# Kernel tuning notes

Hardware: AMD Instinct MI355X
Metric: run time of the kernel (lower is better)

## Reference

```python
import jax, jax.numpy as jnp
import numpy as np

NUM_HEADS = 16
THETA = 10000.0


def _rope(x, cos, sin):
    # x: [B, H, S, d_k]; cos/sin: [S, d_k//2] broadcast over B, H
    x1 = x[..., 0::2]
    x2 = x[..., 1::2]
    r1 = cos * x1 - sin * x2
    r2 = sin * x1 + cos * x2
    # interleave back: (..., half_d, 2) -> (..., d_k)
    return jnp.stack((r1, r2), axis=-1).reshape(x.shape)


def setup_inputs() -> dict:
    key = jax.random.key(0)
    ks = jax.random.split(key, 5)
    B, S, D = 4, 2048, 1024
    scale = D ** -0.5
    x = jax.random.normal(ks[0], (B, S, D), dtype=jnp.float32)
    wq = jax.random.normal(ks[1], (D, D), dtype=jnp.float32) * scale
    wk = jax.random.normal(ks[2], (D, D), dtype=jnp.float32) * scale
    wv = jax.random.normal(ks[3], (D, D), dtype=jnp.float32) * scale
    wo = jax.random.normal(ks[4], (D, D), dtype=jnp.float32) * scale
    return {"x": x, "wq": wq, "wk": wk, "wv": wv, "wo": wo}


def reference(x, wq, wk, wv, wo):
    B, S, D = x.shape
    H = NUM_HEADS
    dk = D // H

    def proj(w):
        # x @ w.T, split heads -> [B, H, S, dk]
        y = jnp.einsum('bsd,ed->bse', x, w)
        return y.reshape(B, S, H, dk).transpose(0, 2, 1, 3)

    q, k, v = proj(wq), proj(wk), proj(wv)

    # RoPE (interleaved pairs), positions = arange(S)
    inv_freq = THETA ** (-(jnp.arange(0, dk, 2, dtype=jnp.float32) / dk))
    ang = jnp.arange(S, dtype=jnp.float32)[:, None] * inv_freq  # [S, dk//2]
    cos, sin = jnp.cos(ang), jnp.sin(ang)
    q = _rope(q, cos, sin)
    k = _rope(k, cos, sin)

    scores = jnp.einsum('bhqd,bhkd->bhqk', q, k) / jnp.sqrt(jnp.asarray(dk, x.dtype))
    causal = jnp.tril(jnp.ones((S, S), dtype=bool))  # keep self + past
    scores = jnp.where(causal, scores, -jnp.inf)
    p = jax.nn.softmax(scores, axis=-1)
    attn = jnp.einsum('bhqk,bhkd->bhqd', p, v)
    attn = attn.transpose(0, 2, 1, 3).reshape(B, S, D)
    return jnp.einsum('bsd,ed->bse', attn, wo)
```

## Files before the change

### kernel.cpp

```cpp
#include <hip/hip_runtime.h>
#include <hip/hip_bf16.h>
#include <cstdint>
#include <cstddef>

#define Bb 4
#define Ss 2048
#define Dd 1024
#define Hh 16
#define Mm (Bb*Ss)

typedef __bf16 bf16_t;
typedef __bf16 bf16x8 __attribute__((ext_vector_type(8)));
typedef __bf16 bf16x4 __attribute__((ext_vector_type(4)));
typedef float  f32x4  __attribute__((ext_vector_type(4)));
typedef float  f32x16 __attribute__((ext_vector_type(16)));
typedef unsigned int u32x4 __attribute__((ext_vector_type(4)));
typedef unsigned int u32x2 __attribute__((ext_vector_type(2)));

#define MFMA16(a,b,c) __builtin_amdgcn_mfma_f32_16x16x32_bf16(a,b,c,0,0,0)
#define MFMA32(a,b,c) __builtin_amdgcn_mfma_f32_32x32x16_bf16(a,b,c,0,0,0)

static __device__ __forceinline__ float fexp2(float x) {
#if __has_builtin(__builtin_amdgcn_exp2f)
  return __builtin_amdgcn_exp2f(x);
#else
  return exp2f(x);
#endif
}

static __device__ __forceinline__ bf16x8 ld16g(const bf16_t* p) {
  return __builtin_bit_cast(bf16x8, *reinterpret_cast<const u32x4*>(p));
}

static __device__ __forceinline__ void gload_lds16(const bf16_t* g, bf16_t* l) {
  __builtin_amdgcn_global_load_lds(
      (__attribute__((address_space(1))) void*)(g),
      (__attribute__((address_space(3))) void*)(l),
      16, 0, 0);
}

__global__ void cvt_f32_bf16(const float* __restrict__ in, bf16_t* __restrict__ out) {
  int i = (blockIdx.x * blockDim.x + threadIdx.x) * 4;
  float4 f = *reinterpret_cast<const float4*>(in + i);
  out[i + 0] = (bf16_t)f.x;
  out[i + 1] = (bf16_t)f.y;
  out[i + 2] = (bf16_t)f.z;
  out[i + 3] = (bf16_t)f.w;
}

__global__ void cvt_w4(const float* __restrict__ w0, const float* __restrict__ w1,
                       const float* __restrict__ w2, const float* __restrict__ w3,
                       bf16_t* __restrict__ out) {
  int bid = blockIdx.x;
  int seg = bid >> 10, local = bid & 1023;
  const float* w = (seg == 0) ? w0 : (seg == 1) ? w1 : (seg == 2) ? w2 : w3;
  int i = (local * 256 + threadIdx.x) * 4;
  float4 f = *reinterpret_cast<const float4*>(w + i);
  bf16_t* o = out + (size_t)seg * (Dd * Dd) + i;
  o[0] = (bf16_t)f.x; o[1] = (bf16_t)f.y; o[2] = (bf16_t)f.z; o[3] = (bf16_t)f.w;
}

template <typename OutT>
__global__ __launch_bounds__(256) void gemm_bt(const bf16_t* __restrict__ A,
                                               const bf16_t* __restrict__ Bm,
                                               OutT* __restrict__ C0,
                                               OutT* __restrict__ C1,
                                               OutT* __restrict__ C2,
                                               int Kdim) {
  __shared__ bf16_t As[2][128 * 32];
  __shared__ bf16_t Bs[2][128 * 32];
  const int t = threadIdx.x;
  const int lane = t & 63, w = t >> 6;
  const int l15 = lane & 15, lg = lane >> 4;
  const int m0 = blockIdx.x * 128, n0 = blockIdx.y * 128;
  const int wr = w >> 1, wc = w & 1;

  f32x4 acc[4][4] = {};

  auto stage = [&](int buf, int kt) {
    const int k0 = kt * 32;
#pragma unroll
    for (int c = 0; c < 2; ++c) {
      int flat = (c * 256 + t) * 16;
      int row = flat >> 6;
      int ke = (flat & 63) >> 1;
      const bf16_t* ga = A  + (size_t)(m0 + row) * Kdim + k0 + ke;
      const bf16_t* gb = Bm + (size_t)(n0 + row) * Kdim + k0 + ke;
      bf16_t* la = &As[buf][c * 2048 + w * 512];
      bf16_t* lb = &Bs[buf][c * 2048 + w * 512];
      gload_lds16(ga, la);
      gload_lds16(gb, lb);
    }
  };

  const int KT = Kdim / 32;
  stage(0, 0);
  __syncthreads();
  int buf = 0;
  for (int kt = 0; kt < KT; ++kt) {
    if (kt + 1 < KT) stage(buf ^ 1, kt + 1);
    bf16x8 af[4], bfr[4];
#pragma unroll
    for (int i = 0; i < 4; ++i) {
      af[i]  = __builtin_bit_cast(bf16x8, *reinterpret_cast<const u32x4*>(
                  &As[buf][(wr * 64 + i * 16 + l15) * 32 + lg * 8]));
      bfr[i] = __builtin_bit_cast(bf16x8, *reinterpret_cast<const u32x4*>(
                  &Bs[buf][(wc * 64 + i * 16 + l15) * 32 + lg * 8]));
    }
#pragma unroll
    for (int i = 0; i < 4; ++i)
#pragma unroll
      for (int j = 0; j < 4; ++j)
        acc[i][j] = MFMA16(af[i], bfr[j], acc[i][j]);
    __syncthreads();
    buf ^= 1;
  }

  OutT* Cs = (n0 < 1024) ? C0 : (n0 < 2048 ? C1 : C2);
  const int nb = n0 & 1023;
#pragma unroll
  for (int i = 0; i < 4; ++i) {
    int rowb = m0 + wr * 64 + i * 16 + lg * 4;
#pragma unroll
    for (int j = 0; j < 4; ++j) {
      int col = nb + wc * 64 + j * 16 + l15;
#pragma unroll
      for (int r = 0; r < 4; ++r)
        Cs[(size_t)(rowb + r) * 1024 + col] = (OutT)acc[i][j][r];
    }
  }
}

__global__ void rope_tab_k(float2* __restrict__ tab) {
  int idx = blockIdx.x * 256 + threadIdx.x;
  int i = idx & 31, s = idx >> 5;
  float inv_freq = exp2f(-(float)i * (13.2877123795494f / 32.0f));
  float ang = (float)s * inv_freq;
  float sn, cs;
  sincosf(ang, &sn, &cs);
  tab[idx] = make_float2(cs, sn);
}

__global__ void rope_apply_k(bf16_t* __restrict__ Q, bf16_t* __restrict__ K,
                             const float2* __restrict__ tab) {
  int tid = blockIdx.x * 256 + threadIdx.x;
  bf16_t* base = blockIdx.y ? K : Q;
  const float scale = blockIdx.y ? 1.0f : 0.18033688011112042f;
  size_t e0 = (size_t)tid * 16;
  int d0 = (int)(e0 & 63);
  int i0 = d0 >> 1;
  int s = (int)((e0 >> 10) & (Ss - 1));
  bf16x8 lo = *reinterpret_cast<const bf16x8*>(base + e0);
  bf16x8 hi = *reinterpret_cast<const bf16x8*>(base + e0 + 8);
  const float2* tb = tab + s * 32 + i0;
  bf16x8 olo, ohi;
#pragma unroll
  for (int j = 0; j < 4; ++j) {
    float2 f = tb[j];
    float x1 = (float)lo[2 * j], x2 = (float)lo[2 * j + 1];
    olo[2 * j]     = (bf16_t)((f.x * x1 - f.y * x2) * scale);
    olo[2 * j + 1] = (bf16_t)((f.y * x1 + f.x * x2) * scale);
  }
#pragma unroll
  for (int j = 0; j < 4; ++j) {
    float2 f = tb[4 + j];
    float x1 = (float)hi[2 * j], x2 = (float)hi[2 * j + 1];
    ohi[2 * j]     = (bf16_t)((f.x * x1 - f.y * x2) * scale);
    ohi[2 * j + 1] = (bf16_t)((f.y * x1 + f.x * x2) * scale);
  }
  *reinterpret_cast<bf16x8*>(base + e0)     = olo;
  *reinterpret_cast<bf16x8*>(base + e0 + 8) = ohi;
}

__global__ __launch_bounds__(256) void transpose_v(const bf16_t* __restrict__ V,
                                                   bf16_t* __restrict__ Vt) {
  __shared__ bf16_t tile[64][72];
  int bh = blockIdx.y;
  int b = bh >> 4, h = bh & 15;
  int s0 = blockIdx.x * 64;
  int t = threadIdx.x;
  const bf16_t* vbase = V + (size_t)b * Ss * Dd + h * 64;
#pragma unroll
  for (int c = 0; c < 2; ++c) {
    int cf = c * 256 + t;
    int s = cf >> 3, d8 = cf & 7;
    u32x4 v = *reinterpret_cast<const u32x4*>(vbase + (size_t)(s0 + s) * Dd + d8 * 8);
    *reinterpret_cast<u32x4*>(&tile[s][d8 * 8]) = v;
  }
  __syncthreads();
  bf16_t* obase = Vt + (size_t)bh * 64 * Ss;
#pragma unroll
  for (int c = 0; c < 2; ++c) {
    int cf = c * 256 + t;
    int d = cf >> 3, s8 = cf & 7;
    __align__(16) bf16_t tmp[8];
#pragma unroll
    for (int i = 0; i < 8; ++i) tmp[i] = tile[s8 * 8 + i][d];
    *reinterpret_cast<u32x4*>(obase + (size_t)d * Ss + s0 + s8 * 8) =
        *reinterpret_cast<const u32x4*>(tmp);
  }
}

__global__ __launch_bounds__(256, 2) void attn_k(const bf16_t* __restrict__ Q,
                                                 const bf16_t* __restrict__ K,
                                                 const bf16_t* __restrict__ Vt,
                                                 bf16_t* __restrict__ O) {
  __shared__ bf16_t Ks[2][2048];
  __shared__ bf16_t Vs[2][2048];
  const int t = threadIdx.x, lane = t & 63, w = t >> 6;
  const int l31 = lane & 31, hi = lane >> 5, hi8 = hi * 8;
  const int bh = blockIdx.y, b = bh >> 4, h = bh & 15;
  const int i = blockIdx.x * 4 + w;
  const int q0a = 32 * i, q0b = 2016 - 32 * i;
  const bf16_t* qb = Q + (size_t)b * Ss * Dd + h * 64;
  const bf16_t* kb = K + (size_t)b * Ss * Dd + h * 64;
  const bf16_t* vtb = Vt + (size_t)bh * 64 * Ss;

  const int a_ = l31 >> 2, c_ = l31 & 3;
  const int tau = (a_ >> 1) + 2 * (a_ & 1) + ((a_ & 4) >> 1);
  const int sig = c_ + 4 * tau;

  int kfoff[4];
#pragma unroll
  for (int c = 0; c < 4; ++c) {
    int j = sig >> 1, u = (sig & 1) * 8 + c * 2 + hi;
    kfoff[c] = j * 128 + ((u ^ j) * 8);
  }
  int vfoff[2][2];
#pragma unroll
  for (int db = 0; db < 2; ++db)
#pragma unroll
    for (int ks = 0; ks < 2; ++ks) {
      int d = db * 32 + l31, j = d >> 2, u = (d & 3) * 4 + ks * 2 + hi;
      vfoff[db][ks] = j * 128 + ((u ^ j) * 8);
    }

  const int sj = t >> 4, ss = t & 15, su = ss ^ sj;
  const bf16_t* ksrc0 = kb + (size_t)(2 * sj + (su >> 3)) * Dd + (su & 7) * 8;
  const bf16_t* vsrc0 = vtb + (size_t)(4 * sj + (su >> 2)) * Ss + (su & 3) * 8;
  bf16_t* kdst = (bf16_t*)Ks[0] + w * 512;
  bf16_t* vdst = (bf16_t*)Vs[0] + w * 512;

  auto stage = [&](int buf, int kbase) {
    gload_lds16(ksrc0 + (size_t)kbase * Dd, kdst + buf * 2048);
    gload_lds16(vsrc0 + kbase,              vdst + buf * 2048);
  };

  bf16x8 qf[2][4];
#pragma unroll
  for (int c = 0; c < 4; ++c) {
    qf[0][c] = ld16g(qb + (size_t)(q0a + l31) * Dd + c * 16 + hi8);
    qf[1][c] = ld16g(qb + (size_t)(q0b + l31) * Dd + c * 16 + hi8);
  }

  float m_[2] = {-INFINITY, -INFINITY};
  float l_[2] = {0.f, 0.f};
  f32x16 o_[2][2] = {};
  const int myNt = 64 - i;
  const int NT = 64 - blockIdx.x * 4;

  stage(0, 0);
  __syncthreads();

  for (int kt = 0; kt < NT; ++kt) {
    const int buf = kt & 1;
    if (kt + 1 < NT) stage(buf ^ 1, (kt + 1) * 32);

    if (kt < myNt) {
      const int kbase = kt * 32;
      bf16x8 kf[4], vf[2][2];
      const bf16_t* kbuf = Ks[buf];
      const bf16_t* vbuf = Vs[buf];
#pragma unroll
      for (int c = 0; c < 4; ++c)
        kf[c] = __builtin_bit_cast(bf16x8,
                  *reinterpret_cast<const u32x4*>(kbuf + kfoff[c]));
#pragma unroll
      for (int db = 0; db < 2; ++db)
#pragma unroll
        for (int ks = 0; ks < 2; ++ks)
          vf[db][ks] = __builtin_bit_cast(bf16x8,
                  *reinterpret_cast<const u32x4*>(vbuf + vfoff[db][ks]));

#pragma unroll
      for (int ch = 0; ch < 2; ++ch) {
        if (ch == 0 && kt > i) continue;
        const bool diag = (ch == 0) ? (kt == i) : (kt == myNt - 1);
        f32x16 s = {};
        __builtin_amdgcn_s_setprio(1);
        s = MFMA32(kf[0], qf[ch][0], s);
        s = MFMA32(kf[1], qf[ch][1], s);
        s = MFMA32(kf[2], qf[ch][2], s);
        s = MFMA32(kf[3], qf[ch][3], s);
        __builtin_amdgcn_s_setprio(0);
        if (diag) {
#pragma unroll
          for (int reg = 0; reg < 16; ++reg) {
            const int koff = (reg & 3) + 4 * (reg >> 2) + 8 * ((reg >> 2) >> 1) + hi8;
            s[reg] = (koff <= l31) ? s[reg] : -INFINITY;
          }
        }
        float px[8];
#pragma unroll
        for (int r = 0; r < 8; ++r) px[r] = fmaxf(s[r], s[r + 8]);
#pragma unroll
        for (int st = 4; st > 0; st >>= 1)
#pragma unroll
          for (int r = 0; r < st; ++r) px[r] = fmaxf(px[r], px[r + st]);
        float pmax = fmaxf(px[0], __shfl_xor(px[0], 32));
        if (!__all(pmax <= m_[ch] + 11.5f)) {
          const float mnew = fmaxf(m_[ch], pmax);
          const float alpha = fexp2(m_[ch] - mnew);
          l_[ch] *= alpha;
          o_[ch][0] *= alpha;
          o_[ch][1] *= alpha;
          m_[ch] = mnew;
        }
        float p[16];
#pragma unroll
        for (int reg = 0; reg < 16; ++reg) p[reg] = fexp2(s[reg] - m_[ch]);
        bf16x8 pb1, pb2;
#pragma unroll
        for (int reg = 0; reg < 8; ++reg) { pb1[reg] = (bf16_t)p[reg];
                                            pb2[reg] = (bf16_t)p[reg + 8]; }
#pragma unroll
        for (int st = 8; st > 0; st >>= 1)
#pragma unroll
          for (int r = 0; r < st; ++r) p[r] += p[r + st];
        l_[ch] += p[0];
        __builtin_amdgcn_s_setprio(1);
        o_[ch][0] = MFMA32(vf[0][0], pb1, o_[ch][0]);
        o_[ch][0] = MFMA32(vf[0][1], pb2, o_[ch][0]);
        o_[ch][1] = MFMA32(vf[1][0], pb1, o_[ch][1]);
        o_[ch][1] = MFMA32(vf[1][1], pb2, o_[ch][1]);
        __builtin_amdgcn_s_setprio(0);
      }
    }
    __syncthreads();
  }

#pragma unroll
  for (int ch = 0; ch < 2; ++ch) {
    const float ltot = l_[ch] + __shfl_xor(l_[ch], 32);
    const float inv = 1.0f / ltot;
    const size_t rowoff = ((size_t)b * Ss + (ch ? q0b : q0a) + l31) * Dd + h * 64;
#pragma unroll
    for (int db = 0; db < 2; ++db)
#pragma unroll
      for (int tt = 0; tt < 4; ++tt) {
        bf16x4 ov;
#pragma unroll
        for (int c = 0; c < 4; ++c) ov[c] = (bf16_t)(o_[ch][db][4 * tt + c] * inv);
        *reinterpret_cast<u32x2*>(&O[rowoff + db * 32 + 8 * tt + 4 * hi]) =
            __builtin_bit_cast(u32x2, ov);
      }
  }
}

extern "C" void kernel_launch(void* const* d_in, const int* in_sizes, int n_in,
                              void* d_out, int out_size, void* d_ws, size_t ws_size,
                              hipStream_t stream) {
  (void)in_sizes; (void)n_in; (void)out_size; (void)ws_size;
  const float* x  = (const float*)d_in[0];
  const float* wq = (const float*)d_in[1];
  const float* wk = (const float*)d_in[2];
  const float* wv = (const float*)d_in[3];
  const float* wo = (const float*)d_in[4];
  float* out = (float*)d_out;

  char* ws = (char*)d_ws;
  const size_t MB16 = 16u << 20;
  bf16_t* xb   = (bf16_t*)(ws + 0);
  bf16_t* Qb   = (bf16_t*)(ws + 1 * MB16);
  bf16_t* Kb   = (bf16_t*)(ws + 2 * MB16);
  bf16_t* Vb   = (bf16_t*)(ws + 3 * MB16);
  bf16_t* wqkv = (bf16_t*)(ws + 4 * MB16);
  bf16_t* wob  = wqkv + 3u * Dd * Dd;
  float2* tab  = (float2*)xb;
  bf16_t* Vt   = xb;
  bf16_t* AOb  = Vb;

  cvt_f32_bf16<<<(Mm * Dd) / 1024, 256, 0, stream>>>(x, xb);
  cvt_w4<<<4096, 256, 0, stream>>>(wq, wk, wv, wo, wqkv);

  gemm_bt<bf16_t><<<dim3(Mm / 128, 24), 256, 0, stream>>>(xb, wqkv, Qb, Kb, Vb, Dd);

  rope_tab_k<<<256, 256, 0, stream>>>(tab);
  rope_apply_k<<<dim3(2048, 2), 256, 0, stream>>>(Qb, Kb, tab);

  transpose_v<<<dim3(Ss / 64, Bb * Hh), 256, 0, stream>>>(Vb, Vt);

  attn_k<<<dim3(8, Bb * Hh), 256, 0, stream>>>(Qb, Kb, Vt, AOb);

  gemm_bt<float><<<dim3(Mm / 128, 8), 256, 0, stream>>>(AOb, wob, out, out, out, Dd);
}
```

Baseline: 192.6 us.

## Use 64-key tiles with triple-buffered LDS pipeline in attention kernel

Each iteration of the causal attention loop now processes 64 keys (two 32-key subtiles) instead of 32, halving the iteration and barrier count and doing one online-softmax rescale per 64 keys. K/V staging moves from double to triple buffering with explicit vmcnt waits, so loads are issued two tiles ahead and only a raw s_barrier is used. LDS per block triples and register pressure rises from holding two K and V fragment sets, which may reduce occupancy under the 256x2 launch bounds.

```diff
diff --git a/kernel.cpp b/kernel.cpp
--- a/kernel.cpp
+++ b/kernel.cpp
@@ -205,13 +205,17 @@
                                                  const bf16_t* __restrict__ K,
                                                  const bf16_t* __restrict__ Vt,
                                                  bf16_t* __restrict__ O) {
-  __shared__ bf16_t Ks[2][2048];
-  __shared__ bf16_t Vs[2][2048];
+  __shared__ bf16_t Ks[3][4096];
+  __shared__ bf16_t Vs[3][4096];
   const int t = threadIdx.x, lane = t & 63, w = t >> 6;
   const int l31 = lane & 31, hi = lane >> 5, hi8 = hi * 8;
   const int bh = blockIdx.y, b = bh >> 4, h = bh & 15;
-  const int i = blockIdx.x * 4 + w;
+  const int bx = blockIdx.x;
+  const int i = bx * 4 + w;
   const int q0a = 32 * i, q0b = 2016 - 32 * i;
+  const int dtA = q0a >> 6, hfA = (q0a >> 5) & 1;
+  const int dtB = q0b >> 6, hfB = (q0b >> 5) & 1;
+  const int NT = 32 - 2 * bx;
   const bf16_t* qb = Q + (size_t)b * Ss * Dd + h * 64;
   const bf16_t* kb = K + (size_t)b * Ss * Dd + h * 64;
   const bf16_t* vtb = Vt + (size_t)bh * 64 * Ss;
@@ -238,12 +242,14 @@
   const int sj = t >> 4, ss = t & 15, su = ss ^ sj;
   const bf16_t* ksrc0 = kb + (size_t)(2 * sj + (su >> 3)) * Dd + (su & 7) * 8;
   const bf16_t* vsrc0 = vtb + (size_t)(4 * sj + (su >> 2)) * Ss + (su & 3) * 8;
-  bf16_t* kdst = (bf16_t*)Ks[0] + w * 512;
-  bf16_t* vdst = (bf16_t*)Vs[0] + w * 512;
-
-  auto stage = [&](int buf, int kbase) {
-    gload_lds16(ksrc0 + (size_t)kbase * Dd, kdst + buf * 2048);
-    gload_lds16(vsrc0 + kbase,              vdst + buf * 2048);
+
+  auto stage = [&](int buf, int kb0) {
+    bf16_t* kd = &Ks[buf][w * 512];
+    bf16_t* vd = &Vs[buf][w * 512];
+    gload_lds16(ksrc0 + (size_t)kb0 * Dd, kd);
+    gload_lds16(ksrc0 + (size_t)(kb0 + 32) * Dd, kd + 2048);
+    gload_lds16(vsrc0 + kb0, vd);
+    gload_lds16(vsrc0 + kb0 + 32, vd + 2048);
   };
 
   bf16x8 qf[2][4];
@@ -256,87 +262,124 @@
   float m_[2] = {-INFINITY, -INFINITY};
   float l_[2] = {0.f, 0.f};
   f32x16 o_[2][2] = {};
-  const int myNt = 64 - i;
-  const int NT = 64 - blockIdx.x * 4;
+
+  auto chain = [&](int kt, int dt, int hf, bf16x8 (&qc)[4],
+                   f32x16& o0, f32x16& o1, float& mc, float& lc,
+                   bf16x8 (&kf)[2][4], bf16x8 (&vf)[2][2][2]) {
+    if (kt > dt) return;
+    const bool last = (kt == dt);
+    const bool do1 = !(last && hf == 0);
+    f32x16 s0 = {}, s1 = {};
+    __builtin_amdgcn_s_setprio(1);
+    s0 = MFMA32(kf[0][0], qc[0], s0);
+    s0 = MFMA32(kf[0][1], qc[1], s0);
+    s0 = MFMA32(kf[0][2], qc[2], s0);
+    s0 = MFMA32(kf[0][3], qc[3], s0);
+    if (do1) {
+      s1 = MFMA32(kf[1][0], qc[0], s1);
+      s1 = MFMA32(kf[1][1], qc[1], s1);
+      s1 = MFMA32(kf[1][2], qc[2], s1);
+      s1 = MFMA32(kf[1][3], qc[3], s1);
+    }
+    __builtin_amdgcn_s_setprio(0);
+    if (last) {
+      if (hf) {
+#pragma unroll
+        for (int reg = 0; reg < 16; ++reg) {
+          const int koff = (reg & 3) + 4 * (reg >> 2) + 8 * ((reg >> 2) >> 1) + hi8;
+          s1[reg] = (koff <= l31) ? s1[reg] : -INFINITY;
+        }
+      } else {
+#pragma unroll
+        for (int reg = 0; reg < 16; ++reg) {
+          const int koff = (reg & 3) + 4 * (reg >> 2) + 8 * ((reg >> 2) >> 1) + hi8;
+          s0[reg] = (koff <= l31) ? s0[reg] : -INFINITY;
+        }
+      }
+    }
+    float px[16];
+    if (do1) {
+#pragma unroll
+      for (int r = 0; r < 16; ++r) px[r] = fmaxf(s0[r], s1[r]);
+    } else {
+#pragma unroll
+      for (int r = 0; r < 16; ++r) px[r] = s0[r];
+    }
+#pragma unroll
+    for (int st2 = 8; st2 > 0; st2 >>= 1)
+#pragma unroll
+      for (int r = 0; r < st2; ++r) px[r] = fmaxf(px[r], px[r + st2]);
+    const float pmax = fmaxf(px[0], __shfl_xor(px[0], 32));
+    if (!__all(pmax <= mc + 11.5f)) {
+      const float mnew = fmaxf(mc, pmax);
+      const float alpha = fexp2(mc - mnew);
+      lc *= alpha;
+      o0 *= alpha;
+      o1 *= alpha;
+      mc = mnew;
+    }
+    float p0[16], p1[16];
+#pragma unroll
+    for (int r = 0; r < 16; ++r) p0[r] = fexp2(s0[r] - mc);
+    bf16x8 pa0, pa1, pb0, pb1;
+#pragma unroll
+    for (int r = 0; r < 8; ++r) { pa0[r] = (bf16_t)p0[r]; pa1[r] = (bf16_t)p0[r + 8]; }
+    if (do1) {
+#pragma unroll
+      for (int r = 0; r < 16; ++r) p1[r] = fexp2(s1[r] - mc);
+#pragma unroll
+      for (int r = 0; r < 8; ++r) { pb0[r] = (bf16_t)p1[r]; pb1[r] = (bf16_t)p1[r + 8]; }
+#pragma unroll
+      for (int r = 0; r < 16; ++r) p0[r] += p1[r];
+    }
+#pragma unroll
+    for (int st2 = 8; st2 > 0; st2 >>= 1)
+#pragma unroll
+      for (int r = 0; r < st2; ++r) p0[r] += p0[r + st2];
+    lc += p0[0];
+    __builtin_amdgcn_s_setprio(1);
+    o0 = MFMA32(vf[0][0][0], pa0, o0);
+    o0 = MFMA32(vf[0][0][1], pa1, o0);
+    o1 = MFMA32(vf[0][1][0], pa0, o1);
+    o1 = MFMA32(vf[0][1][1], pa1, o1);
+    if (do1) {
+      o0 = MFMA32(vf[1][0][0], pb0, o0);
+      o0 = MFMA32(vf[1][0][1], pb1, o0);
+      o1 = MFMA32(vf[1][1][0], pb0, o1);
+      o1 = MFMA32(vf[1][1][1], pb1, o1);
+    }
+    __builtin_amdgcn_s_setprio(0);
+  };
 
   stage(0, 0);
-  __syncthreads();
-
-  for (int kt = 0; kt < NT; ++kt) {
-    const int buf = kt & 1;
-    if (kt + 1 < NT) stage(buf ^ 1, (kt + 1) * 32);
-
-    if (kt < myNt) {
-      const int kbase = kt * 32;
-      bf16x8 kf[4], vf[2][2];
-      const bf16_t* kbuf = Ks[buf];
-      const bf16_t* vbuf = Vs[buf];
+  stage(1, 64);
+  for (int j = 0; j < NT; ++j) {
+    if (j == NT - 1) {
+      asm volatile("s_waitcnt vmcnt(0) lgkmcnt(0)" ::: "memory");
+    } else {
+      asm volatile("s_waitcnt vmcnt(4) lgkmcnt(0)" ::: "memory");
+    }
+    __builtin_amdgcn_s_barrier();
+    if (j + 2 < NT) stage((j + 2) % 3, (j + 2) * 64);
+    const bf16_t* kbuf = &Ks[j % 3][0];
+    const bf16_t* vbuf = &Vs[j % 3][0];
+    bf16x8 kf[2][4], vf[2][2][2];
+#pragma unroll
+    for (int st = 0; st < 2; ++st)
 #pragma unroll
       for (int c = 0; c < 4; ++c)
-        kf[c] = __builtin_bit_cast(bf16x8,
-                  *reinterpret_cast<const u32x4*>(kbuf + kfoff[c]));
+        kf[st][c] = __builtin_bit_cast(bf16x8,
+            *reinterpret_cast<const u32x4*>(kbuf + st * 2048 + kfoff[c]));
+#pragma unroll
+    for (int st = 0; st < 2; ++st)
 #pragma unroll
       for (int db = 0; db < 2; ++db)
 #pragma unroll
         for (int ks = 0; ks < 2; ++ks)
-          vf[db][ks] = __builtin_bit_cast(bf16x8,
-                  *reinterpret_cast<const u32x4*>(vbuf + vfoff[db][ks]));
-
-#pragma unroll
-      for (int ch = 0; ch < 2; ++ch) {
-        if (ch == 0 && kt > i) continue;
-        const bool diag = (ch == 0) ? (kt == i) : (kt == myNt - 1);
-        f32x16 s = {};
-        __builtin_amdgcn_s_setprio(1);
-        s = MFMA32(kf[0], qf[ch][0], s);
-        s = MFMA32(kf[1], qf[ch][1], s);
-        s = MFMA32(kf[2], qf[ch][2], s);
-        s = MFMA32(kf[3], qf[ch][3], s);
-        __builtin_amdgcn_s_setprio(0);
-        if (diag) {
-#pragma unroll
-          for (int reg = 0; reg < 16; ++reg) {
-            const int koff = (reg & 3) + 4 * (reg >> 2) + 8 * ((reg >> 2) >> 1) + hi8;
-            s[reg] = (koff <= l31) ? s[reg] : -INFINITY;
-          }
-        }
-        float px[8];
-#pragma unroll
-        for (int r = 0; r < 8; ++r) px[r] = fmaxf(s[r], s[r + 8]);
-#pragma unroll
-        for (int st = 4; st > 0; st >>= 1)
-#pragma unroll
-          for (int r = 0; r < st; ++r) px[r] = fmaxf(px[r], px[r + st]);
-        float pmax = fmaxf(px[0], __shfl_xor(px[0], 32));
-        if (!__all(pmax <= m_[ch] + 11.5f)) {
-          const float mnew = fmaxf(m_[ch], pmax);
-          const float alpha = fexp2(m_[ch] - mnew);
-          l_[ch] *= alpha;
-          o_[ch][0] *= alpha;
-          o_[ch][1] *= alpha;
-          m_[ch] = mnew;
-        }
-        float p[16];
-#pragma unroll
-        for (int reg = 0; reg < 16; ++reg) p[reg] = fexp2(s[reg] - m_[ch]);
-        bf16x8 pb1, pb2;
-#pragma unroll
-        for (int reg = 0; reg < 8; ++reg) { pb1[reg] = (bf16_t)p[reg];
-                                            pb2[reg] = (bf16_t)p[reg + 8]; }
-#pragma unroll
-        for (int st = 8; st > 0; st >>= 1)
-#pragma unroll
-          for (int r = 0; r < st; ++r) p[r] += p[r + st];
-        l_[ch] += p[0];
-        __builtin_amdgcn_s_setprio(1);
-        o_[ch][0] = MFMA32(vf[0][0], pb1, o_[ch][0]);
-        o_[ch][0] = MFMA32(vf[0][1], pb2, o_[ch][0]);
-        o_[ch][1] = MFMA32(vf[1][0], pb1, o_[ch][1]);
-        o_[ch][1] = MFMA32(vf[1][1], pb2, o_[ch][1]);
-        __builtin_amdgcn_s_setprio(0);
-      }
-    }
-    __syncthreads();
+          vf[st][db][ks] = __builtin_bit_cast(bf16x8,
+              *reinterpret_cast<const u32x4*>(vbuf + st * 2048 + vfoff[db][ks]));
+    chain(j, dtA, hfA, qf[0], o_[0][0], o_[0][1], m_[0], l_[0], kf, vf);
+    chain(j, dtB, hfB, qf[1], o_[1][0], o_[1][1], m_[1], l_[1], kf, vf);
   }
 
 #pragma unroll
```

After: 188.5 us. 1.02x faster.
